# Optimization experiments

Measured on AMD Instinct MI355X. Metric: run time of the kernel, lower is better.

## Reference

```python
import jax, jax.numpy as jnp
import numpy as np

RHO = 100.0
W = 256
CHUNK = 64 * 64  # pixel tile size, as in the torch render loop


def _rot_matrices():
    # eulers ('zyx') used by the module; each has only one nonzero angle so
    # the scipy intrinsic/extrinsic distinction is moot.
    def Ry(t):
        c, s = np.cos(t), np.sin(t)
        return np.array([[c, 0, s], [0, 1, 0], [-s, 0, c]])

    def Rx(t):
        c, s = np.cos(t), np.sin(t)
        return np.array([[1, 0, 0], [0, c, -s], [0, s, c]])

    p = np.pi
    mats = [np.eye(3), Ry(p / 2), Ry(p), Ry(3 * p / 2), Rx(p / 2), Rx(3 * p / 2)]
    return np.stack(mats).astype(np.float32)  # [6,3,3]


def _pix_xy():
    idx = np.arange(W * W)
    i, j = idx // W, idx % W
    pix = np.stack([j, i], axis=1).astype(np.float32)  # [W2,2] (x=col, y=row)
    return (pix - W // 2 + 0.5) / (W // 2)


def _render(x, src_n, pix_chunks):
    # x: [N,3] rotated points; pix_chunks: [n_chunks, CHUNK, 2]
    depth = x[:, 2]
    dmin = jax.lax.stop_gradient(jnp.min(depth))  # torch uses .item() -> constant
    dmax = jax.lax.stop_gradient(jnp.max(depth))
    pix_val = 1.0 - (depth - dmin) / (dmax - dmin)  # [N]
    xy = x[:, :2]

    def chunk_fn(pxy):  # pxy: [CHUNK,2]
        d2 = jnp.sum((xy[:, None, :] - pxy[None, :, :]) ** 2, axis=-1)  # [N,CHUNK]
        wgt = jnp.exp(-d2 / 2 * RHO ** 2)
        v = pix_val[:, None] * wgt
        return jnp.max(v[:src_n], axis=0), jnp.max(v[src_n:], axis=0)

    src_img, tgt_img = jax.lax.map(jax.checkpoint(chunk_fn), pix_chunks)
    return jnp.stack([src_img.reshape(W, W), tgt_img.reshape(W, W)], axis=0)  # [2,W,W]


def setup_inputs() -> dict:
    key = jax.random.key(0)
    k1, k2 = jax.random.split(key)
    src_pred = jax.random.normal(k1, (4096, 3), dtype=jnp.float32)
    tgt_pcd = jax.random.normal(k2, (4096, 3), dtype=jnp.float32)
    return {"src_pred": src_pred, "tgt_pcd": tgt_pcd}


def reference(src_pred, tgt_pcd):
    rots = jnp.asarray(_rot_matrices())          # [6,3,3]
    pix_xy = jnp.asarray(_pix_xy())              # [W2,2]
    pix_chunks = pix_xy.reshape(-1, CHUNK, 2)    # [n_chunks, CHUNK, 2]
    registrated = jnp.concatenate([src_pred, tgt_pcd], axis=0)  # [N,3]
    src_n = src_pred.shape[0]
    imgs = []
    for v in range(rots.shape[0]):
        x = registrated @ rots[v].T  # == (rot @ pts.T).T
        img = _render(x, src_n, pix_chunks)
        imgs.append((img - 0.5) / 0.5)
    return jnp.stack(imgs, axis=0)  # [6,2,W,W]
```

## Files before the change

kernel.cpp:

```cpp
#include <hip/hip_runtime.h>
#include <math.h>


#define WIMG 256
#define HALF 4096
#define CLOG2 7213.475204444817f
#define INV_CLOG2 1.3862943611198906e-4f
#define RCUT 0.084f
#define SCAP 2048

static __device__ __constant__ float RMAT[6][9] = {
  { 1.f, 0.f, 0.f,   0.f, 1.f, 0.f,   0.f, 0.f, 1.f },
  { 6.123233995736766e-17f, 0.f, 1.f,  0.f, 1.f, 0.f,  -1.f, 0.f, 6.123233995736766e-17f },
  { -1.f, 0.f, 1.2246467991473532e-16f, 0.f, 1.f, 0.f, -1.2246467991473532e-16f, 0.f, -1.f },
  { -1.8369701987210297e-16f, 0.f, -1.f, 0.f, 1.f, 0.f,  1.f, 0.f, -1.8369701987210297e-16f },
  { 1.f, 0.f, 0.f,  0.f, 6.123233995736766e-17f, -1.f,  0.f, 1.f, 6.123233995736766e-17f },
  { 1.f, 0.f, 0.f,  0.f, -1.8369701987210297e-16f, 1.f, 0.f, -1.f, -1.8369701987210297e-16f },
};

__global__ __launch_bounds__(256) void fused_render(const float* __restrict__ src,
                                                    const float* __restrict__ tgt,
                                                    float* __restrict__ out) {
  __shared__ float4 sc[SCAP];
  __shared__ float smin[4], smax[4];
  __shared__ int s_n;

  const int b = blockIdx.x;
  const int vh = b >> 6;
  const int tile = (b + 21 * vh) & 63;
  const int v = vh >> 1, h = vh & 1;
  const int tx = tile & 3, ty = tile >> 2;
  const int col0 = tx << 6, row0 = ty << 4;
  const int tid = threadIdx.x;
  const int lane = tid & 63, w = tid >> 6;

  const float* R = RMAT[v];
  const float r00 = R[0], r01 = R[1], r02 = R[2];
  const float r10 = R[3], r11 = R[4], r12 = R[5];
  const float r20 = R[6], r21 = R[7], r22 = R[8];

  const float* own = h ? tgt : src;
  const float* oth = h ? src : tgt;
  float zmin = 3.0e38f, zmax = -3.0e38f;
  float xs[16], ys[16], zs[16];
#pragma unroll
  for (int j = 0; j < 16; ++j) {
    const float* p = oth + 3 * (tid + 256 * j);
    const float a = p[0], bb = p[1], c = p[2];
    const float z = r20 * a + r21 * bb + r22 * c;
    zmin = fminf(zmin, z);
    zmax = fmaxf(zmax, z);
  }
#pragma unroll
  for (int j = 0; j < 16; ++j) {
    const float* p = own + 3 * (tid + 256 * j);
    const float a = p[0], bb = p[1], c = p[2];
    const float z = r20 * a + r21 * bb + r22 * c;
    zmin = fminf(zmin, z);
    zmax = fmaxf(zmax, z);
    xs[j] = r00 * a + r01 * bb + r02 * c;
    ys[j] = r10 * a + r11 * bb + r12 * c;
    zs[j] = z;
  }
#pragma unroll
  for (int off = 32; off > 0; off >>= 1) {
    zmin = fminf(zmin, __shfl_down(zmin, off));
    zmax = fmaxf(zmax, __shfl_down(zmax, off));
  }
  if (tid == 0) s_n = 0;
  if (lane == 0) { smin[w] = zmin; smax[w] = zmax; }
  __syncthreads();
  const float dmin = fminf(fminf(smin[0], smin[1]), fminf(smin[2], smin[3]));
  const float dmax = fmaxf(fmaxf(smax[0], smax[1]), fmaxf(smax[2], smax[3]));
  const float range = dmax - dmin;

  const float pxmin = (col0 - 127.5f) * 0.0078125f;
  const float pymin = (row0 - 127.5f) * 0.0078125f;
  const float bx0 = pxmin - RCUT, bx1 = pxmin + 63.0f * 0.0078125f + RCUT;
  const float by0 = pymin - RCUT, by1 = pymin + 15.0f * 0.0078125f + RCUT;
#pragma unroll
  for (int j = 0; j < 16; ++j) {
    const float x = xs[j], y = ys[j];
    if (x >= bx0 && x <= bx1 && y >= by0 && y <= by1) {
      const float pv = 1.0f - (zs[j] - dmin) / range;
      const float pen = (pv > 0.f) ? (-log2f(pv) * INV_CLOG2) : 1.0e26f;
      const int idx = atomicAdd(&s_n, 1);
      if (idx < SCAP) sc[idx] = make_float4(x, y, pen, 0.f);
    }
  }
  __syncthreads();
  const int total = min(s_n, SCAP);

  const float px  = (col0 + lane - 127.5f) * 0.0078125f;
  const float py0 = (row0 + w - 127.5f) * 0.0078125f;
  const float py1 = py0 + 0.03125f;
  const float py2 = py0 + 0.0625f;
  const float py3 = py0 + 0.09375f;
  float m0 = 3.0e38f, m1 = 3.0e38f, m2 = 3.0e38f, m3 = 3.0e38f;
  int k = 0;
  for (; k + 1 < total; k += 2) {
    const float4 A = sc[k];
    const float4 B = sc[k + 1];
    const float dxa = A.x - px; const float ca = fmaf(dxa, dxa, A.z);
    const float dxb = B.x - px; const float cb = fmaf(dxb, dxb, B.z);
    float da, db;
    da = A.y - py0; db = B.y - py0;
    m0 = fminf(fminf(m0, fmaf(da, da, ca)), fmaf(db, db, cb));
    da = A.y - py1; db = B.y - py1;
    m1 = fminf(fminf(m1, fmaf(da, da, ca)), fmaf(db, db, cb));
    da = A.y - py2; db = B.y - py2;
    m2 = fminf(fminf(m2, fmaf(da, da, ca)), fmaf(db, db, cb));
    da = A.y - py3; db = B.y - py3;
    m3 = fminf(fminf(m3, fmaf(da, da, ca)), fmaf(db, db, cb));
  }
  if (k < total) {
    const float4 A = sc[k];
    const float dxa = A.x - px; const float ca = fmaf(dxa, dxa, A.z);
    float da;
    da = A.y - py0; m0 = fminf(m0, fmaf(da, da, ca));
    da = A.y - py1; m1 = fminf(m1, fmaf(da, da, ca));
    da = A.y - py2; m2 = fminf(m2, fmaf(da, da, ca));
    da = A.y - py3; m3 = fminf(m3, fmaf(da, da, ca));
  }

  float* o = out + (vh * WIMG + row0 + w) * WIMG + col0 + lane;
  o[0]    = 2.0f * exp2f(-CLOG2 * m0) - 1.0f;
  o[1024] = 2.0f * exp2f(-CLOG2 * m1) - 1.0f;
  o[2048] = 2.0f * exp2f(-CLOG2 * m2) - 1.0f;
  o[3072] = 2.0f * exp2f(-CLOG2 * m3) - 1.0f;
}

extern "C" void kernel_launch(void* const* d_in, const int* in_sizes, int n_in,
                              void* d_out, int out_size, void* d_ws, size_t ws_size,
                              hipStream_t stream) {
  const float* src = (const float*)d_in[0];
  const float* tgt = (const float*)d_in[1];
  float* out = (float*)d_out;
  (void)d_ws; (void)ws_size;
  fused_render<<<768, 256, 0, stream>>>(src, tgt, out);
}
```

Measured before the change: 69.73 us.

## Split point transform and depth normalization into a separate prep kernel

Adds a prep kernel that rotates all points per view, computes the depth min/max once and writes float4 (x, y, penalty) records to workspace. The render kernel then just loads precomputed records and culls per tile, so 768 blocks no longer each redo the 8192-point transform, reduction and log2. It also halves the shared-memory capacity to 1024 entries, which may raise occupancy. The cost is a second launch and a prep stage that runs on only 6 blocks, and a tile holding more than 1024 candidate points would silently drop some.

```diff
diff --git a/kernel.cpp b/kernel.cpp
--- a/kernel.cpp
+++ b/kernel.cpp
@@ -3,11 +3,12 @@
 
 
 #define WIMG 256
+#define NPTS 8192
 #define HALF 4096
 #define CLOG2 7213.475204444817f
 #define INV_CLOG2 1.3862943611198906e-4f
 #define RCUT 0.084f
-#define SCAP 2048
+#define SCAP 1024
 
 static __device__ __constant__ float RMAT[6][9] = {
   { 1.f, 0.f, 0.f,   0.f, 1.f, 0.f,   0.f, 0.f, 1.f },
@@ -18,11 +19,51 @@
   { 1.f, 0.f, 0.f,  0.f, -1.8369701987210297e-16f, 1.f, 0.f, -1.f, -1.8369701987210297e-16f },
 };
 
-__global__ __launch_bounds__(256) void fused_render(const float* __restrict__ src,
-                                                    const float* __restrict__ tgt,
-                                                    float* __restrict__ out) {
+__global__ __launch_bounds__(256) void prep_kernel(const float* __restrict__ src,
+                                                   const float* __restrict__ tgt,
+                                                   float4* __restrict__ pts) {
+  const int v = blockIdx.x;
+  const int tid = threadIdx.x;
+  const float* R = RMAT[v];
+  const float r20 = R[6], r21 = R[7], r22 = R[8];
+
+  float zmin = 3.0e38f, zmax = -3.0e38f;
+  for (int i = tid; i < NPTS; i += 256) {
+    const float* p = (i < HALF) ? (src + 3 * i) : (tgt + 3 * (i - HALF));
+    const float z = r20 * p[0] + r21 * p[1] + r22 * p[2];
+    zmin = fminf(zmin, z);
+    zmax = fmaxf(zmax, z);
+  }
+#pragma unroll
+  for (int off = 32; off > 0; off >>= 1) {
+    zmin = fminf(zmin, __shfl_down(zmin, off));
+    zmax = fmaxf(zmax, __shfl_down(zmax, off));
+  }
+  __shared__ float smin[4], smax[4];
+  const int lane = tid & 63, w = tid >> 6;
+  if (lane == 0) { smin[w] = zmin; smax[w] = zmax; }
+  __syncthreads();
+  const float dmin = fminf(fminf(smin[0], smin[1]), fminf(smin[2], smin[3]));
+  const float dmax = fmaxf(fmaxf(smax[0], smax[1]), fmaxf(smax[2], smax[3]));
+  const float range = dmax - dmin;
+
+  const float r00 = R[0], r01 = R[1], r02 = R[2];
+  const float r10 = R[3], r11 = R[4], r12 = R[5];
+  for (int i = tid; i < NPTS; i += 256) {
+    const float* p = (i < HALF) ? (src + 3 * i) : (tgt + 3 * (i - HALF));
+    const float a = p[0], bb = p[1], c = p[2];
+    const float x = r00 * a + r01 * bb + r02 * c;
+    const float y = r10 * a + r11 * bb + r12 * c;
+    const float z = r20 * a + r21 * bb + r22 * c;
+    const float pv = 1.0f - (z - dmin) / range;
+    const float pen = (pv > 0.f) ? (-log2f(pv) * INV_CLOG2) : 1.0e26f;
+    pts[v * NPTS + i] = make_float4(x, y, pen, 0.f);
+  }
+}
+
+__global__ __launch_bounds__(256) void render_tile(const float4* __restrict__ pts,
+                                                   float* __restrict__ out) {
   __shared__ float4 sc[SCAP];
-  __shared__ float smin[4], smax[4];
   __shared__ int s_n;
 
   const int b = blockIdx.x;
@@ -34,58 +75,21 @@
   const int tid = threadIdx.x;
   const int lane = tid & 63, w = tid >> 6;
 
-  const float* R = RMAT[v];
-  const float r00 = R[0], r01 = R[1], r02 = R[2];
-  const float r10 = R[3], r11 = R[4], r12 = R[5];
-  const float r20 = R[6], r21 = R[7], r22 = R[8];
-
-  const float* own = h ? tgt : src;
-  const float* oth = h ? src : tgt;
-  float zmin = 3.0e38f, zmax = -3.0e38f;
-  float xs[16], ys[16], zs[16];
-#pragma unroll
-  for (int j = 0; j < 16; ++j) {
-    const float* p = oth + 3 * (tid + 256 * j);
-    const float a = p[0], bb = p[1], c = p[2];
-    const float z = r20 * a + r21 * bb + r22 * c;
-    zmin = fminf(zmin, z);
-    zmax = fmaxf(zmax, z);
-  }
-#pragma unroll
-  for (int j = 0; j < 16; ++j) {
-    const float* p = own + 3 * (tid + 256 * j);
-    const float a = p[0], bb = p[1], c = p[2];
-    const float z = r20 * a + r21 * bb + r22 * c;
-    zmin = fminf(zmin, z);
-    zmax = fmaxf(zmax, z);
-    xs[j] = r00 * a + r01 * bb + r02 * c;
-    ys[j] = r10 * a + r11 * bb + r12 * c;
-    zs[j] = z;
-  }
-#pragma unroll
-  for (int off = 32; off > 0; off >>= 1) {
-    zmin = fminf(zmin, __shfl_down(zmin, off));
-    zmax = fmaxf(zmax, __shfl_down(zmax, off));
-  }
   if (tid == 0) s_n = 0;
-  if (lane == 0) { smin[w] = zmin; smax[w] = zmax; }
   __syncthreads();
-  const float dmin = fminf(fminf(smin[0], smin[1]), fminf(smin[2], smin[3]));
-  const float dmax = fmaxf(fmaxf(smax[0], smax[1]), fmaxf(smax[2], smax[3]));
-  const float range = dmax - dmin;
 
   const float pxmin = (col0 - 127.5f) * 0.0078125f;
   const float pymin = (row0 - 127.5f) * 0.0078125f;
   const float bx0 = pxmin - RCUT, bx1 = pxmin + 63.0f * 0.0078125f + RCUT;
   const float by0 = pymin - RCUT, by1 = pymin + 15.0f * 0.0078125f + RCUT;
+
+  const float4* base = pts + v * NPTS + h * HALF;
 #pragma unroll
   for (int j = 0; j < 16; ++j) {
-    const float x = xs[j], y = ys[j];
-    if (x >= bx0 && x <= bx1 && y >= by0 && y <= by1) {
-      const float pv = 1.0f - (zs[j] - dmin) / range;
-      const float pen = (pv > 0.f) ? (-log2f(pv) * INV_CLOG2) : 1.0e26f;
+    const float4 q = base[tid + 256 * j];
+    if (q.x >= bx0 && q.x <= bx1 && q.y >= by0 && q.y <= by1) {
       const int idx = atomicAdd(&s_n, 1);
-      if (idx < SCAP) sc[idx] = make_float4(x, y, pen, 0.f);
+      if (idx < SCAP) sc[idx] = q;
     }
   }
   __syncthreads();
@@ -136,6 +140,8 @@
   const float* src = (const float*)d_in[0];
   const float* tgt = (const float*)d_in[1];
   float* out = (float*)d_out;
-  (void)d_ws; (void)ws_size;
-  fused_render<<<768, 256, 0, stream>>>(src, tgt, out);
+  float4* pts = (float4*)d_ws;
+
+  prep_kernel<<<6, 256, 0, stream>>>(src, tgt, pts);
+  render_tile<<<768, 256, 0, stream>>>(pts, out);
 }
```

Measured after the change: 86.76 us. 1.24x slower.
